# Kernel optimization log

Measured on AMD Instinct MI355X. Metric: run time of the kernel, lower is better.

Reference implementation:

```python
import jax, jax.numpy as jnp
import numpy as np

B, L, D, H = 4, 2048, 1024, 16
DK = D // H  # 64


def setup_inputs() -> dict:
    key = jax.random.key(0)
    ks = jax.random.split(key, 5)
    scale = 1.0 / np.sqrt(D)
    return {
        "x": jax.random.normal(ks[0], (B, L, D), dtype=jnp.float32),
        "Wq": jax.random.normal(ks[1], (D, D), dtype=jnp.float32) * scale,
        "Wk": jax.random.normal(ks[2], (D, D), dtype=jnp.float32) * scale,
        "Wv": jax.random.normal(ks[3], (D, D), dtype=jnp.float32) * scale,
        "Wo": jax.random.normal(ks[4], (D, D), dtype=jnp.float32) * scale,
    }


def reference(x, Wq, Wk, Wv, Wo):
    b, l, d = x.shape
    # Linear: y = x @ W^T (weight stored as [out, in], no bias)
    def proj(W):
        y = jnp.einsum('bld,ed->ble', x, W)            # [B,L,D]
        return y.reshape(b, l, H, DK).transpose(0, 2, 1, 3)  # [B,H,L,dk]
    Q, K, V = proj(Wq), proj(Wk), proj(Wv)
    scores = jnp.einsum('bhqd,bhkd->bhqk', Q, K) / jnp.sqrt(jnp.float32(DK))
    causal = jnp.tril(jnp.ones((l, l), dtype=bool))
    scores = jnp.where(causal[None, None, :, :], scores, jnp.float32(-1e30))
    attn = jax.nn.softmax(scores, axis=-1)             # stable softmax
    out = jnp.einsum('bhqk,bhkd->bhqd', attn, V)       # [B,H,L,dk]
    out = out.transpose(0, 2, 1, 3).reshape(b, l, d)   # [B,L,D]
    return jnp.einsum('bld,ed->ble', out, Wo)
```

## Files before the change

### kernel.cpp

```cpp
#include <hip/hip_runtime.h>
#include <hip/hip_bf16.h>
#include <stdint.h>

typedef short bf16x8 __attribute__((ext_vector_type(8)));
typedef float f32x4 __attribute__((ext_vector_type(4)));
typedef float f32x16 __attribute__((ext_vector_type(16)));
typedef unsigned int uint4v __attribute__((ext_vector_type(4)));

#define NB 4
#define NL 2048
#define ND 1024
#define NH 16
#define NDK 64
#define NM (NB*NL)
#define QSCALE 0.18033688011112042f

__device__ __forceinline__ ushort f2bf(float f) {
  __bf16 h = (__bf16)f;
  return __builtin_bit_cast(unsigned short, h);
}

__device__ __forceinline__ unsigned int cvtpk(float lo, float hi) {
  unsigned int d;
  asm("v_cvt_pk_bf16_f32 %0, %1, %2" : "=v"(d) : "v"(lo), "v"(hi));
  return d;
}

__device__ __forceinline__ void gload16(const void* g, void* l) {
  __builtin_amdgcn_global_load_lds(
      (__attribute__((address_space(1))) void*)(uintptr_t)g,
      (__attribute__((address_space(3))) void*)(uint32_t)(uintptr_t)l,
      16, 0, 0);
}

__device__ __forceinline__ f32x16 mfma32(bf16x8 a, bf16x8 b, f32x16 c) {
  return __builtin_amdgcn_mfma_f32_32x32x16_bf16(a, b, c, 0, 0, 0);
}
__device__ __forceinline__ f32x4 mfma16(bf16x8 a, bf16x8 b, f32x4 c) {
  return __builtin_amdgcn_mfma_f32_16x16x32_bf16(a, b, c, 0, 0, 0);
}

__global__ void convert_all(const float* __restrict__ x, const float* __restrict__ wq,
                            const float* __restrict__ wk, const float* __restrict__ wv,
                            const float* __restrict__ wo, ushort* __restrict__ o) {
  long i = (long)blockIdx.x * 256 + threadIdx.x;
  const long NX = 2097152;
  const long NW = 262144;
  const float4* s;
  long off;
  if (i < NX) { s = (const float4*)x; off = i; }
  else {
    long j = i - NX;
    int wsel = (int)(j >> 18);
    off = j & (NW - 1);
    s = (const float4*)(wsel == 0 ? wq : wsel == 1 ? wk : wsel == 2 ? wv : wo);
  }
  float4 v = s[off];
  ushort4 r;
  r.x = f2bf(v.x); r.y = f2bf(v.y); r.z = f2bf(v.z); r.w = f2bf(v.w);
  ((ushort4*)o)[i] = r;
}

template<int MODE>
__global__ __launch_bounds__(256, 2)
void gemm_bt(const ushort* __restrict__ A,
             const ushort* __restrict__ Bq, const ushort* __restrict__ Bk, const ushort* __restrict__ Bv,
             ushort* __restrict__ Oq, ushort* __restrict__ Ok, ushort* __restrict__ Ov,
             float* __restrict__ OF) {
  __shared__ __align__(16) ushort lA[2][128 * 32];
  __shared__ __align__(16) ushort lB[2][128 * 32];
  const int t = threadIdx.x;
  const int w = t >> 6, l = t & 63;
  const int lr = l & 15, lh = l >> 4;
  const int bxr = blockIdx.x;
  const int bx = (bxr & 7) * 8 + (bxr >> 3);
  const int m0 = bx * 128;
  const int ng = blockIdx.y * 128;
  const ushort* Bp;
  ushort* Op = nullptr;
  int mi = 0, n0;
  if (MODE == 0) {
    mi = ng >> 10;
    Bp = (mi == 0) ? Bq : (mi == 1) ? Bk : Bv;
    Op = (mi == 0) ? Oq : (mi == 1) ? Ok : Ov;
    n0 = ng & 1023;
  } else {
    Bp = Bq;
    n0 = ng;
  }
  const int wrow = (w >> 1) * 64, wcol = (w & 1) * 64;
  const int r = t >> 2, c = t & 3;
  const ushort* gA0 = A + (size_t)(m0 + r) * ND + c * 8;
  const ushort* gA1 = A + (size_t)(m0 + 64 + r) * ND + c * 8;
  const ushort* gB0 = Bp + (size_t)(n0 + r) * ND + c * 8;
  const ushort* gB1 = Bp + (size_t)(n0 + 64 + r) * ND + c * 8;

#define GSTAGE(bi, kofs) do {                              \
    gload16(gA0 + (kofs), &lA[bi][w * 512]);               \
    gload16(gA1 + (kofs), &lA[bi][2048 + w * 512]);        \
    gload16(gB0 + (kofs), &lB[bi][w * 512]);               \
    gload16(gB1 + (kofs), &lB[bi][2048 + w * 512]);        \
  } while (0)

  GSTAGE(0, 0);
  f32x4 acc[4][4] = {};
  for (int kt = 0; kt < ND; kt += 32) {
    const int buf = (kt >> 5) & 1;
    __syncthreads();
    if (kt + 32 < ND) GSTAGE(buf ^ 1, kt + 32);
    bf16x8 af[4], bfr[4];
#pragma unroll
    for (int mt = 0; mt < 4; mt++)
      af[mt] = *(const bf16x8*)&lA[buf][(wrow + mt * 16 + lr) * 32 + lh * 8];
#pragma unroll
    for (int nt = 0; nt < 4; nt++)
      bfr[nt] = *(const bf16x8*)&lB[buf][(wcol + nt * 16 + lr) * 32 + lh * 8];
#pragma unroll
    for (int mt = 0; mt < 4; mt++)
#pragma unroll
      for (int nt = 0; nt < 4; nt++)
        acc[mt][nt] = mfma16(af[mt], bfr[nt], acc[mt][nt]);
  }
#undef GSTAGE
#pragma unroll
  for (int mt = 0; mt < 4; mt++) {
#pragma unroll
    for (int nt = 0; nt < 4; nt++) {
#pragma unroll
      for (int j = 0; j < 4; j++) {
        int m = m0 + wrow + mt * 16 + lh * 4 + j;
        int n = wcol + nt * 16 + lr;
        if (MODE == 0) {
          int nl = n0 + n;
          int b = m >> 11, ll = m & 2047;
          int h = nl >> 6, dk = nl & 63;
          float v = acc[mt][nt][j];
          if (mi == 0) v *= QSCALE;
          if (mi == 2)
            Op[(((size_t)(b * NH + h)) * NDK + dk) * NL + ll] = f2bf(v);
          else
            Op[(((size_t)(b * NH + h)) * NL + ll) * NDK + dk] = f2bf(v);
        } else {
          OF[(size_t)m * ND + ng + n] = acc[mt][nt][j];
        }
      }
    }
  }
}

__global__ __launch_bounds__(256, 4)
void attn_fwd(const ushort* __restrict__ Q, const ushort* __restrict__ Kg,
              const ushort* __restrict__ VT, ushort* __restrict__ O) {
  __shared__ __align__(16) ushort lK[2][64 * 64];
  __shared__ __align__(16) ushort lV[2][64 * 64];
  const int t = threadIdx.x;
  const int w = t >> 6, l = t & 63;
  const int l31 = l & 31, hi = l >> 5;
  const int id = blockIdx.x;
  const int bh = id & 63;
  const int g = (id >> 6) & 3;
  const int k4 = id >> 8;
  const int qt = (k4 == 0) ? g : (k4 == 1) ? 7 - g : (k4 == 2) ? 8 + g : 15 - g;
  const size_t base = (size_t)bh * (NL * NDK);
  const int q0w = qt * 128 + w * 32;
  const int ktmax = q0w >> 6;
  const int NT = qt * 2 + 2;

  bf16x8 qf[4];
  {
    const ushort* qp = Q + base + (size_t)(q0w + l31) * NDK + hi * 8;
#pragma unroll
    for (int sl = 0; sl < 4; sl++) qf[sl] = *(const bf16x8*)(qp + sl * 16);
  }
  bf16x8 ones;
#pragma unroll
  for (int r = 0; r < 8; r++) ones[r] = (short)0x3F80;

  const int kr0 = t >> 3, kc0 = (t & 7) ^ (kr0 & 7);
  const int s1i = t + 256;
  const int kr1 = s1i >> 3, kc1 = (s1i & 7) ^ (kr1 & 7);
  const ushort* gK0 = Kg + base + (size_t)kr0 * NDK + kc0 * 8;
  const ushort* gK1 = Kg + base + (size_t)kr1 * NDK + kc1 * 8;
  const ushort* gV0 = VT + base + (size_t)kr0 * NL + kc0 * 8;
  const ushort* gV1 = VT + base + (size_t)kr1 * NL + kc1 * 8;

  f32x16 accO0 = {}, accO1 = {}, accS = {};
  const int swz = l31 & 7;

#define STAGE(bufi, kt1) do {                                       \
    const size_t kvn = (size_t)(kt1) * 64;                          \
    gload16(gK0 + kvn * NDK, &lK[bufi][w * 512]);                   \
    gload16(gK1 + kvn * NDK, &lK[bufi][2048 + w * 512]);            \
    gload16(gV0 + kvn, &lV[bufi][w * 512]);                         \
    gload16(gV1 + kvn, &lV[bufi][2048 + w * 512]);                  \
  } while (0)

  STAGE(0, 0);

  for (int kt = 0; kt < NT; kt++) {
    const int buf = kt & 1;
    __syncthreads();
    if (kt + 1 < NT) STAGE(buf ^ 1, kt + 1);
    if (kt <= ktmax) {
      const int kv0 = kt * 64;
      const ushort* bK = lK[buf];
      const ushort* bV = lV[buf];
      f32x16 s0 = {}, s1v = {};
      __builtin_amdgcn_s_setprio(1);
#pragma unroll
      for (int sl = 0; sl < 4; sl++) {
        int c = 2 * sl + hi;
        bf16x8 kf0 = *(const bf16x8*)&bK[l31 * 64 + ((c ^ swz) * 8)];
        bf16x8 kf1 = *(const bf16x8*)&bK[(32 + l31) * 64 + ((c ^ swz) * 8)];
        s0 = mfma32(kf0, qf[sl], s0);
        s1v = mfma32(kf1, qf[sl], s1v);
      }
      __builtin_amdgcn_s_setprio(0);
      if (kt == ktmax) {
        const int qrel = q0w + l31 - kv0;
#pragma unroll
        for (int r = 0; r < 16; r++) {
          int kvo = (r & 3) + 8 * (r >> 2) + 4 * hi;
          if (kvo > qrel) s0[r] = -1e30f;
          if (kvo + 32 > qrel) s1v[r] = -1e30f;
        }
      }
#pragma unroll
      for (int r = 0; r < 16; r++) s0[r] = exp2f(s0[r]);
#pragma unroll
      for (int r = 0; r < 16; r++) s1v[r] = exp2f(s1v[r]);
      bf16x8 pa[4];
#pragma unroll
      for (int ks = 0; ks < 4; ks++) {
        const int k2 = (ks & 1) * 8;
        unsigned int a0, a1, b0, b1;
        if (ks >> 1) {
          a0 = cvtpk(s1v[k2 + 0], s1v[k2 + 1]); a1 = cvtpk(s1v[k2 + 2], s1v[k2 + 3]);
          b0 = cvtpk(s1v[k2 + 4], s1v[k2 + 5]); b1 = cvtpk(s1v[k2 + 6], s1v[k2 + 7]);
        } else {
          a0 = cvtpk(s0[k2 + 0], s0[k2 + 1]); a1 = cvtpk(s0[k2 + 2], s0[k2 + 3]);
          b0 = cvtpk(s0[k2 + 4], s0[k2 + 5]); b1 = cvtpk(s0[k2 + 6], s0[k2 + 7]);
        }
        unsigned int a0s = __shfl_xor(a0, 32), a1s = __shfl_xor(a1, 32);
        unsigned int b0s = __shfl_xor(b0, 32), b1s = __shfl_xor(b1, 32);
        uint4v pd;
        pd[0] = hi ? b0s : a0;
        pd[1] = hi ? b1s : a1;
        pd[2] = hi ? b0 : a0s;
        pd[3] = hi ? b1 : a1s;
        pa[ks] = __builtin_bit_cast(bf16x8, pd);
      }
      __builtin_amdgcn_s_setprio(1);
#pragma unroll
      for (int ks = 0; ks < 4; ks++) {
        int c = 2 * ks + hi;
        bf16x8 vf0 = *(const bf16x8*)&bV[l31 * 64 + ((c ^ swz) * 8)];
        bf16x8 vf1 = *(const bf16x8*)&bV[(32 + l31) * 64 + ((c ^ swz) * 8)];
        accO0 = mfma32(vf0, pa[ks], accO0);
        accO1 = mfma32(vf1, pa[ks], accO1);
        accS = mfma32(ones, pa[ks], accS);
      }
      __builtin_amdgcn_s_setprio(0);
    }
  }
#undef STAGE
  const int b = bh >> 4, h = bh & 15;
  const float inv = 1.0f / accS[0];
  const int q = q0w + l31;
  ushort* orow = O + ((size_t)b * NL + q) * ND + h * NDK;
#pragma unroll
  for (int gi = 0; gi < 4; gi++) {
    ushort4 o0, o1;
    o0.x = f2bf(accO0[4 * gi + 0] * inv); o0.y = f2bf(accO0[4 * gi + 1] * inv);
    o0.z = f2bf(accO0[4 * gi + 2] * inv); o0.w = f2bf(accO0[4 * gi + 3] * inv);
    o1.x = f2bf(accO1[4 * gi + 0] * inv); o1.y = f2bf(accO1[4 * gi + 1] * inv);
    o1.z = f2bf(accO1[4 * gi + 2] * inv); o1.w = f2bf(accO1[4 * gi + 3] * inv);
    *(ushort4*)&orow[8 * gi + 4 * hi] = o0;
    *(ushort4*)&orow[32 + 8 * gi + 4 * hi] = o1;
  }
}

extern "C" void kernel_launch(void* const* d_in, const int* in_sizes, int n_in,
                              void* d_out, int out_size, void* d_ws, size_t ws_size,
                              hipStream_t stream) {
  const float* x = (const float*)d_in[0];
  const float* wq = (const float*)d_in[1];
  const float* wk = (const float*)d_in[2];
  const float* wv = (const float*)d_in[3];
  const float* wo = (const float*)d_in[4];
  char* ws = (char*)d_ws;
  ushort* xb  = (ushort*)(ws);
  ushort* wqb = (ushort*)(ws + 16777216);
  ushort* wkb = (ushort*)(ws + 18874368);
  ushort* wvb = (ushort*)(ws + 20971520);
  ushort* wob = (ushort*)(ws + 23068672);
  ushort* Qb  = (ushort*)(ws + 25165824);
  ushort* Kb  = (ushort*)(ws + 41943040);
  ushort* Vb  = (ushort*)(ws + 58720256);
  ushort* Ob  = (ushort*)(ws + 75497472);

  convert_all<<<12288, 256, 0, stream>>>(x, wq, wk, wv, wo, xb);
  gemm_bt<0><<<dim3(64, 24), 256, 0, stream>>>(xb, wqb, wkb, wvb, Qb, Kb, Vb, nullptr);
  attn_fwd<<<dim3(1024), 256, 0, stream>>>(Qb, Kb, Vb, Ob);
  gemm_bt<1><<<dim3(64, 8), 256, 0, stream>>>(Ob, wob, nullptr, nullptr,
                                              nullptr, nullptr, nullptr, (float*)d_out);
}
```

Baseline: 177.5 us.

## Triple-buffer K/V tiles with vmcnt waits and reorder blocks longest-first

The attention kernel goes from double to triple buffering of K/V tiles in LDS, prefetching two tiles ahead. It replaces __syncthreads with an explicit s_waitcnt vmcnt plus s_barrier, so loads for the next tiles can stay in flight. The block-to-query-tile mapping changes from a balanced interleave to longest-first ordering, so the heaviest causal tiles start first. This uses more LDS per block and lowers the launch-bounds occupancy hint from 4 to 3 blocks, and it relies on the vmcnt counts matching the number of outstanding direct-to-LDS loads.

```diff
diff --git a/kernel.cpp b/kernel.cpp
--- a/kernel.cpp
+++ b/kernel.cpp
@@ -148,19 +148,17 @@
   }
 }
 
-__global__ __launch_bounds__(256, 4)
+__global__ __launch_bounds__(256, 3)
 void attn_fwd(const ushort* __restrict__ Q, const ushort* __restrict__ Kg,
               const ushort* __restrict__ VT, ushort* __restrict__ O) {
-  __shared__ __align__(16) ushort lK[2][64 * 64];
-  __shared__ __align__(16) ushort lV[2][64 * 64];
+  __shared__ __align__(16) ushort lK[3][64 * 64];
+  __shared__ __align__(16) ushort lV[3][64 * 64];
   const int t = threadIdx.x;
   const int w = t >> 6, l = t & 63;
   const int l31 = l & 31, hi = l >> 5;
   const int id = blockIdx.x;
   const int bh = id & 63;
-  const int g = (id >> 6) & 3;
-  const int k4 = id >> 8;
-  const int qt = (k4 == 0) ? g : (k4 == 1) ? 7 - g : (k4 == 2) ? 8 + g : 15 - g;
+  const int qt = 15 - (id >> 6);
   const size_t base = (size_t)bh * (NL * NDK);
   const int q0w = qt * 128 + w * 32;
   const int ktmax = q0w >> 6;
@@ -187,24 +185,28 @@
   f32x16 accO0 = {}, accO1 = {}, accS = {};
   const int swz = l31 & 7;
 
-#define STAGE(bufi, kt1) do {                                       \
+#define STAGE(slot, kt1) do {                                       \
     const size_t kvn = (size_t)(kt1) * 64;                          \
-    gload16(gK0 + kvn * NDK, &lK[bufi][w * 512]);                   \
-    gload16(gK1 + kvn * NDK, &lK[bufi][2048 + w * 512]);            \
-    gload16(gV0 + kvn, &lV[bufi][w * 512]);                         \
-    gload16(gV1 + kvn, &lV[bufi][2048 + w * 512]);                  \
+    gload16(gK0 + kvn * NDK, &lK[slot][w * 512]);                   \
+    gload16(gK1 + kvn * NDK, &lK[slot][2048 + w * 512]);            \
+    gload16(gV0 + kvn, &lV[slot][w * 512]);                         \
+    gload16(gV1 + kvn, &lV[slot][2048 + w * 512]);                  \
   } while (0)
 
   STAGE(0, 0);
-
+  STAGE(1, 1);
+
+  int scur = 0, snxt = 2;
   for (int kt = 0; kt < NT; kt++) {
-    const int buf = kt & 1;
-    __syncthreads();
-    if (kt + 1 < NT) STAGE(buf ^ 1, kt + 1);
+    if (kt + 1 < NT) asm volatile("s_waitcnt vmcnt(4)" ::: "memory");
+    else             asm volatile("s_waitcnt vmcnt(0)" ::: "memory");
+    __builtin_amdgcn_s_barrier();
+    __builtin_amdgcn_sched_barrier(0);
+    if (kt + 2 < NT) STAGE(snxt, kt + 2);
     if (kt <= ktmax) {
       const int kv0 = kt * 64;
-      const ushort* bK = lK[buf];
-      const ushort* bV = lV[buf];
+      const ushort* bK = lK[scur];
+      const ushort* bV = lV[scur];
       f32x16 s0 = {}, s1v = {};
       __builtin_amdgcn_s_setprio(1);
 #pragma unroll
@@ -262,6 +264,8 @@
       }
       __builtin_amdgcn_s_setprio(0);
     }
+    scur = (scur + 1 == 3) ? 0 : scur + 1;
+    snxt = (snxt + 1 == 3) ? 0 : snxt + 1;
   }
 #undef STAGE
   const int b = bh >> 4, h = bh & 15;
```

Measured after the change: 172.3 us. 1.03x faster.
